# Kernel optimization log

Measured on AMD Instinct MI355X. Metric: run time of the kernel, lower is better.

The kernel has to match this reference:

```python
import jax, jax.numpy as jnp
import numpy as np

ROPE_BASE = 10000.0


def apply_rope(x, start_pos):
    # x: (b, s, n, d) -- interleaved-pair rotary embedding (LLaMA style)
    b, s, n, d = x.shape
    inv_freq = 1.0 / (ROPE_BASE ** (jnp.arange(0, d, 2, dtype=jnp.float32) / d))  # (d/2,)
    pos = jnp.arange(start_pos, start_pos + s, dtype=jnp.float32)                 # (s,)
    ang = pos[:, None] * inv_freq[None, :]                                        # (s, d/2)
    cos = jnp.cos(ang)[None, :, None, :]  # (1, s, 1, d/2)
    sin = jnp.sin(ang)[None, :, None, :]
    x1 = x[..., 0::2]
    x2 = x[..., 1::2]
    out = jnp.stack([x1 * cos - x2 * sin, x1 * sin + x2 * cos], axis=-1)
    return out.reshape(b, s, n, d).astype(x.dtype)


def setup_inputs() -> dict:
    key = jax.random.key(0)
    k1, k2, k3, k4 = jax.random.split(key, 4)
    b, n, s, d = 4, 32, 512, 128
    max_b, n_mem = 4, 4096
    return {
        "q": jax.random.normal(k1, (b, n, s, d), dtype=jnp.float32),
        "k": jax.random.normal(k2, (b, n, s, d), dtype=jnp.float32),
        "v": jax.random.normal(k3, (b, n, s, d), dtype=jnp.float32),
        "mem_kv": jax.random.normal(k4, (2, max_b, n_mem, n, d), dtype=jnp.float32),
        "start_pos": 2048,
    }


def reference(q, k, v, mem_kv, start_pos):
    b, n, s, d = q.shape
    # view_in: (b n s d) -> (b s n d)
    q_ = jnp.transpose(q, (0, 2, 1, 3))
    k_ = jnp.transpose(k, (0, 2, 1, 3))
    v_ = jnp.transpose(v, (0, 2, 1, 3))
    # rotary on q, k with absolute positions offset by start_pos
    q_ = apply_rope(q_, start_pos)
    k_ = apply_rope(k_, start_pos)
    # KV-cache write + read
    mem_k = mem_kv[0].at[:b, start_pos:start_pos + s].set(k_)
    mem_v = mem_kv[1].at[:b, start_pos:start_pos + s].set(v_)
    k_full = mem_k[:b, :start_pos + s]  # (b, t, n, d)
    v_full = mem_v[:b, :start_pos + s]
    # view_out: (b s n d) -> (b n s d)
    qh = jnp.transpose(q_, (0, 2, 1, 3))
    kh = jnp.transpose(k_full, (0, 2, 1, 3))
    vh = jnp.transpose(v_full, (0, 2, 1, 3))
    scale = d ** (-0.5)
    sim = jnp.einsum('bnsd,bntd->bnst', qh, kh) * scale
    attn = jax.nn.softmax(sim, axis=-1)
    return jnp.einsum('bnst,bntd->bnsd', attn, vh)
```

## Files before the change

kernel.cpp:

```cpp
#include <hip/hip_runtime.h>

#define BB   4
#define NN   32
#define SS   512
#define DD   128
#define NMEM 4096
#define MAXB 4
#define MQ   64
#define NK   64

typedef __attribute__((ext_vector_type(8))) short short8;
typedef __attribute__((ext_vector_type(4))) short short4v;
typedef __attribute__((ext_vector_type(4))) float f32x4;

__device__ __forceinline__ ushort bf16_rne(float x) {
    unsigned u = __float_as_uint(x);
    return (ushort)((u + 0x7FFFu + ((u >> 16) & 1u)) >> 16);
}

__device__ __forceinline__ void split_bf16(float x, ushort& hi, ushort& lo) {
    ushort hb = bf16_rne(x);
    float hf = __uint_as_float(((unsigned)hb) << 16);
    hi = hb;
    lo = bf16_rne(x - hf);
}

__device__ __forceinline__ void load_kv_row(const float* __restrict__ kg,
                                            const float* __restrict__ vg,
                                            const float* __restrict__ mg,
                                            int batch, int head, int start_pos, int T,
                                            int t, int d0, float nlb,
                                            float* kb, float* vb)
{
    if (t < start_pos) {
        const float* ks = mg + (((long)batch * NMEM + t) * NN + head) * DD + d0;
        const float* vs = ks + (long)MAXB * NMEM * NN * DD;
        float4 kk = *(const float4*)ks;
        float4 vv = *(const float4*)vs;
        kb[0] = kk.x; kb[1] = kk.y; kb[2] = kk.z; kb[3] = kk.w;
        vb[0] = vv.x; vb[1] = vv.y; vb[2] = vv.z; vb[3] = vv.w;
    } else if (t < T) {
        const long off = (((long)(batch * NN + head)) * SS + (t - start_pos)) * DD + d0;
        float4 kk = *(const float4*)(kg + off);
        float4 vv = *(const float4*)(vg + off);
        float sn, cs;
        sincosf((float)t * __expf(nlb * (float)d0), &sn, &cs);
        kb[0] = kk.x * cs - kk.y * sn;
        kb[1] = kk.x * sn + kk.y * cs;
        sincosf((float)t * __expf(nlb * (float)(d0 + 2)), &sn, &cs);
        kb[2] = kk.z * cs - kk.w * sn;
        kb[3] = kk.z * sn + kk.w * cs;
        vb[0] = vv.x; vb[1] = vv.y; vb[2] = vv.z; vb[3] = vv.w;
    } else {
        kb[0] = kb[1] = kb[2] = kb[3] = 0.f;
        vb[0] = vb[1] = vb[2] = vb[3] = 0.f;
    }
}

__global__ __launch_bounds__(256)
void mra_attn_mfma(const float* __restrict__ qg,
                   const float* __restrict__ kg,
                   const float* __restrict__ vg,
                   const float* __restrict__ mg,
                   const int*  __restrict__ spp,
                   float* __restrict__ outg)
{
    const int start_pos = spp[0];
    const int T = start_pos + SS;
    const int ntiles = (T + NK - 1) / NK;

    const int qblk  = blockIdx.x;
    const int head  = blockIdx.y;
    const int batch = blockIdx.z;
    const int tid   = threadIdx.x;
    const int wv    = tid >> 6;
    const int lane  = tid & 63;
    const int h     = lane >> 4;
    const int m     = lane & 15;

    __shared__ ushort khi[NK * DD];
    __shared__ ushort klo[NK * DD];
    __shared__ ushort vts[DD * NK];

    const float nlb   = -9.210340371976184f / 128.0f;
    const float scale = 0.08838834764831845f;

    const int q0 = qblk * MQ;
#pragma unroll
    for (int p = 0; p < 8; ++p) {
        const int idx = p * 1024 + tid * 4;
        const int row = idx >> 7;
        const int col = idx & 127;
        const int pos = start_pos + q0 + row;
        float4 x = *(const float4*)(qg + (((long)(batch * NN + head)) * SS + q0 + row) * DD + col);
        float sn, cs;
        sincosf((float)pos * __expf(nlb * (float)col), &sn, &cs);
        float e0 = (x.x * cs - x.y * sn) * scale;
        float e1 = (x.x * sn + x.y * cs) * scale;
        sincosf((float)pos * __expf(nlb * (float)(col + 2)), &sn, &cs);
        float e2 = (x.z * cs - x.w * sn) * scale;
        float e3 = (x.z * sn + x.w * cs) * scale;
        ushort hh[4], ll[4];
        split_bf16(e0, hh[0], ll[0]);
        split_bf16(e1, hh[1], ll[1]);
        split_bf16(e2, hh[2], ll[2]);
        split_bf16(e3, hh[3], ll[3]);
        *(ushort4*)(&khi[row * DD + col]) = make_ushort4(hh[0], hh[1], hh[2], hh[3]);
        *(ushort4*)(&klo[row * DD + col]) = make_ushort4(ll[0], ll[1], ll[2], ll[3]);
    }
    __syncthreads();

    short8 qfh[4], qfl[4];
    {
        const ushort* qrh = &khi[(wv * 16 + m) * DD];
        const ushort* qrl = &klo[(wv * 16 + m) * DD];
#pragma unroll
        for (int dc = 0; dc < 4; ++dc) {
            qfh[dc] = *(const short8*)(qrh + dc * 32 + h * 8);
            qfl[dc] = *(const short8*)(qrl + dc * 32 + h * 8);
        }
    }
    __syncthreads();

    f32x4 acc[8];
    const f32x4 zero4 = {0.f, 0.f, 0.f, 0.f};
#pragma unroll
    for (int i = 0; i < 8; ++i) acc[i] = zero4;
    float m_run = -1e30f, l_run = 0.f;

    for (int kt = 0; kt < ntiles; ++kt) {
        const int tile0 = kt * NK;

#pragma unroll
        for (int p = 0; p < 4; ++p) {
            const int pi = p * 256 + tid;
            const int d0 = (pi & 31) * 4;
            const int t0 = (pi >> 5) * 2;
            float kA[4], vA[4], kB[4], vB[4];
            load_kv_row(kg, vg, mg, batch, head, start_pos, T, tile0 + t0,     d0, nlb, kA, vA);
            load_kv_row(kg, vg, mg, batch, head, start_pos, T, tile0 + t0 + 1, d0, nlb, kB, vB);
            {
                const int co = d0 ^ ((t0 & 7) << 3);
                ushort hh[4], ll[4];
#pragma unroll
                for (int j = 0; j < 4; ++j) split_bf16(kA[j], hh[j], ll[j]);
                *(ushort4*)(&khi[t0 * DD + co]) = make_ushort4(hh[0], hh[1], hh[2], hh[3]);
                *(ushort4*)(&klo[t0 * DD + co]) = make_ushort4(ll[0], ll[1], ll[2], ll[3]);
            }
            {
                const int t1 = t0 + 1;
                const int co = d0 ^ ((t1 & 7) << 3);
                ushort hh[4], ll[4];
#pragma unroll
                for (int j = 0; j < 4; ++j) split_bf16(kB[j], hh[j], ll[j]);
                *(ushort4*)(&khi[t1 * DD + co]) = make_ushort4(hh[0], hh[1], hh[2], hh[3]);
                *(ushort4*)(&klo[t1 * DD + co]) = make_ushort4(ll[0], ll[1], ll[2], ll[3]);
            }
#pragma unroll
            for (int j = 0; j < 4; ++j) {
                const int d = d0 + j;
                unsigned pk = (unsigned)bf16_rne(vA[j]) | ((unsigned)bf16_rne(vB[j]) << 16);
                *(unsigned*)(&vts[d * NK + (t0 ^ ((d & 15) << 2))]) = pk;
            }
        }
        __syncthreads();

        float sc[16];
#pragma unroll
        for (int c = 0; c < 4; ++c) {
            f32x4 s = zero4;
            const int krow = c * 16 + m;
            const ushort* krh = &khi[krow * DD];
            const ushort* krl = &klo[krow * DD];
            const int sw = (krow & 7) << 3;
#pragma unroll
            for (int dc = 0; dc < 4; ++dc) {
                const int o = (dc * 32 + h * 8) ^ sw;
                short8 kfh = *(const short8*)(krh + o);
                short8 kfl = *(const short8*)(krl + o);
                s = __builtin_amdgcn_mfma_f32_16x16x32_bf16(kfh, qfh[dc], s, 0, 0, 0);
                s = __builtin_amdgcn_mfma_f32_16x16x32_bf16(kfh, qfl[dc], s, 0, 0, 0);
                s = __builtin_amdgcn_mfma_f32_16x16x32_bf16(kfl, qfh[dc], s, 0, 0, 0);
            }
            if (tile0 + NK > T) {
#pragma unroll
                for (int r = 0; r < 4; ++r)
                    if (tile0 + c * 16 + h * 4 + r >= T) s[r] = -1e30f;
            }
#pragma unroll
            for (int r = 0; r < 4; ++r) sc[c * 4 + r] = s[r];
        }

        float mloc = sc[0];
#pragma unroll
        for (int i = 1; i < 16; ++i) mloc = fmaxf(mloc, sc[i]);
        mloc = fmaxf(mloc, __shfl_xor(mloc, 16));
        mloc = fmaxf(mloc, __shfl_xor(mloc, 32));
        const float mnew = fmaxf(m_run, mloc);
        float lloc = 0.f;
#pragma unroll
        for (int i = 0; i < 16; ++i) {
            float pv = __expf(sc[i] - mnew);
            sc[i] = pv;
            lloc += pv;
        }
        lloc += __shfl_xor(lloc, 16);
        lloc += __shfl_xor(lloc, 32);
        const float alpha = __expf(m_run - mnew);
        l_run = l_run * alpha + lloc;
        m_run = mnew;
#pragma unroll
        for (int db = 0; db < 8; ++db) acc[db] = acc[db] * alpha;

#pragma unroll
        for (int g = 0; g < 2; ++g) {
            short8 pf;
#pragma unroll
            for (int j = 0; j < 8; ++j) pf[j] = (short)bf16_rne(sc[g * 8 + j]);
#pragma unroll
            for (int db = 0; db < 8; ++db) {
                const int drow = db * 16 + m;
                const ushort* vr = &vts[drow * NK];
                const int sw = (drow & 15) << 2;
                short4v a0 = *(const short4v*)(vr + ((g * 32 + h * 4) ^ sw));
                short4v a1 = *(const short4v*)(vr + ((g * 32 + 16 + h * 4) ^ sw));
                short8 vf = __builtin_shufflevector(a0, a1, 0, 1, 2, 3, 4, 5, 6, 7);
                acc[db] = __builtin_amdgcn_mfma_f32_16x16x32_bf16(vf, pf, acc[db], 0, 0, 0);
            }
        }
        __syncthreads();
    }

    const float inv_l = 1.f / l_run;
    float* dst = outg + (((long)(batch * NN + head)) * SS + q0 + wv * 16 + m) * DD;
#pragma unroll
    for (int db = 0; db < 8; ++db) {
        float4 o = make_float4(acc[db][0] * inv_l, acc[db][1] * inv_l,
                               acc[db][2] * inv_l, acc[db][3] * inv_l);
        *(float4*)(dst + db * 16 + h * 4) = o;
    }
}

extern "C" void kernel_launch(void* const* d_in, const int* in_sizes, int n_in,
                              void* d_out, int out_size, void* d_ws, size_t ws_size,
                              hipStream_t stream) {
    const float* q      = (const float*)d_in[0];
    const float* k      = (const float*)d_in[1];
    const float* v      = (const float*)d_in[2];
    const float* mem_kv = (const float*)d_in[3];
    const int*   sp     = (const int*)d_in[4];
    float* out = (float*)d_out;

    dim3 grid(SS / MQ, NN, BB);
    dim3 block(256);
    hipLaunchKernelGGL(mra_attn_mfma, grid, block, 0, stream, q, k, v, mem_kv, sp, out);
}
```

Baseline: 1.174 ms.

## Double query tile per block, specialize KV staging by region, remap grid

Raises the query tile from 64 to 128 rows with 512-thread blocks, so each staged K/V tile feeds twice as many queries and global K/V traffic is halved. KV staging is templated into memory-only, new-only and mixed modes, which removes per-row branching and hoists the rope frequencies. Q rope is loaded straight into registers instead of going through LDS. The grid is flattened and remapped so the query blocks of a head run on different dispatch slots. The hi part of the bf16 split is changed to truncation. The trade-off is fewer blocks (512), higher register pressure under launch_bounds(512,4), and the trailing barrier moved to the top of the loop.

Result: faster. 1.031 ms (-12.2%).

```diff
diff --git a/kernel.cpp b/kernel.cpp
--- a/kernel.cpp
+++ b/kernel.cpp
@@ -6,8 +6,9 @@
 #define DD   128
 #define NMEM 4096
 #define MAXB 4
-#define MQ   64
+#define MQ   128
 #define NK   64
+#define VOFF ((long)MAXB * NMEM * NN * DD)
 
 typedef __attribute__((ext_vector_type(8))) short short8;
 typedef __attribute__((ext_vector_type(4))) short short4v;
@@ -19,37 +20,37 @@
 }
 
 __device__ __forceinline__ void split_bf16(float x, ushort& hi, ushort& lo) {
-    ushort hb = bf16_rne(x);
-    float hf = __uint_as_float(((unsigned)hb) << 16);
-    hi = hb;
-    lo = bf16_rne(x - hf);
-}
-
-__device__ __forceinline__ void load_kv_row(const float* __restrict__ kg,
-                                            const float* __restrict__ vg,
-                                            const float* __restrict__ mg,
-                                            int batch, int head, int start_pos, int T,
-                                            int t, int d0, float nlb,
-                                            float* kb, float* vb)
+    unsigned u = __float_as_uint(x);
+    hi = (ushort)(u >> 16);
+    lo = bf16_rne(x - __uint_as_float(u & 0xffff0000u));
+}
+
+template<int MODE>
+__device__ __forceinline__ void fetch_row(const float* __restrict__ kmem,
+                                          const float* __restrict__ knew,
+                                          const float* __restrict__ vnew,
+                                          int t, int start_pos, int T,
+                                          float fr0, float fr2,
+                                          float* kb, float* vb)
 {
-    if (t < start_pos) {
-        const float* ks = mg + (((long)batch * NMEM + t) * NN + head) * DD + d0;
-        const float* vs = ks + (long)MAXB * NMEM * NN * DD;
+    const bool from_mem = (MODE == 0) || (MODE == 2 && t < start_pos);
+    if (from_mem) {
+        const float* ks = kmem + (long)t * (NN * DD);
         float4 kk = *(const float4*)ks;
-        float4 vv = *(const float4*)vs;
+        float4 vv = *(const float4*)(ks + VOFF);
         kb[0] = kk.x; kb[1] = kk.y; kb[2] = kk.z; kb[3] = kk.w;
         vb[0] = vv.x; vb[1] = vv.y; vb[2] = vv.z; vb[3] = vv.w;
-    } else if (t < T) {
-        const long off = (((long)(batch * NN + head)) * SS + (t - start_pos)) * DD + d0;
-        float4 kk = *(const float4*)(kg + off);
-        float4 vv = *(const float4*)(vg + off);
-        float sn, cs;
-        sincosf((float)t * __expf(nlb * (float)d0), &sn, &cs);
-        kb[0] = kk.x * cs - kk.y * sn;
-        kb[1] = kk.x * sn + kk.y * cs;
-        sincosf((float)t * __expf(nlb * (float)(d0 + 2)), &sn, &cs);
-        kb[2] = kk.z * cs - kk.w * sn;
-        kb[3] = kk.z * sn + kk.w * cs;
+    } else if (MODE == 1 || t < T) {
+        const long off = (long)(t - start_pos) * DD;
+        float4 kk = *(const float4*)(knew + off);
+        float4 vv = *(const float4*)(vnew + off);
+        float sn0, cs0, sn2, cs2;
+        sincosf((float)t * fr0, &sn0, &cs0);
+        sincosf((float)t * fr2, &sn2, &cs2);
+        kb[0] = kk.x * cs0 - kk.y * sn0;
+        kb[1] = kk.x * sn0 + kk.y * cs0;
+        kb[2] = kk.z * cs2 - kk.w * sn2;
+        kb[3] = kk.z * sn2 + kk.w * cs2;
         vb[0] = vv.x; vb[1] = vv.y; vb[2] = vv.z; vb[3] = vv.w;
     } else {
         kb[0] = kb[1] = kb[2] = kb[3] = 0.f;
@@ -57,7 +58,49 @@
     }
 }
 
-__global__ __launch_bounds__(256)
+template<int MODE>
+__device__ __forceinline__ void stage_tile(const float* __restrict__ kmem,
+                                           const float* __restrict__ knew,
+                                           const float* __restrict__ vnew,
+                                           int tile0, int start_pos, int T,
+                                           int d0, int tr0, float fr0, float fr2,
+                                           ushort* __restrict__ khi,
+                                           ushort* __restrict__ klo,
+                                           ushort* __restrict__ vts)
+{
+#pragma unroll
+    for (int p = 0; p < 2; ++p) {
+        const int trr = tr0 + p * 32;
+        float kA[4], vA[4], kB[4], vB[4];
+        fetch_row<MODE>(kmem, knew, vnew, tile0 + trr,     start_pos, T, fr0, fr2, kA, vA);
+        fetch_row<MODE>(kmem, knew, vnew, tile0 + trr + 1, start_pos, T, fr0, fr2, kB, vB);
+        {
+            const int co = d0 ^ ((trr & 7) << 3);
+            ushort hh[4], ll[4];
+#pragma unroll
+            for (int j = 0; j < 4; ++j) split_bf16(kA[j], hh[j], ll[j]);
+            *(ushort4*)(&khi[trr * DD + co]) = make_ushort4(hh[0], hh[1], hh[2], hh[3]);
+            *(ushort4*)(&klo[trr * DD + co]) = make_ushort4(ll[0], ll[1], ll[2], ll[3]);
+        }
+        {
+            const int t1 = trr + 1;
+            const int co = d0 ^ ((t1 & 7) << 3);
+            ushort hh[4], ll[4];
+#pragma unroll
+            for (int j = 0; j < 4; ++j) split_bf16(kB[j], hh[j], ll[j]);
+            *(ushort4*)(&khi[t1 * DD + co]) = make_ushort4(hh[0], hh[1], hh[2], hh[3]);
+            *(ushort4*)(&klo[t1 * DD + co]) = make_ushort4(ll[0], ll[1], ll[2], ll[3]);
+        }
+#pragma unroll
+        for (int j = 0; j < 4; ++j) {
+            const int d = d0 + j;
+            unsigned pk = (unsigned)bf16_rne(vA[j]) | ((unsigned)bf16_rne(vB[j]) << 16);
+            *(unsigned*)(&vts[d * NK + (trr ^ ((d & 15) << 2))]) = pk;
+        }
+    }
+}
+
+__global__ __launch_bounds__(512, 4)
 void mra_attn_mfma(const float* __restrict__ qg,
                    const float* __restrict__ kg,
                    const float* __restrict__ vg,
@@ -69,14 +112,18 @@
     const int T = start_pos + SS;
     const int ntiles = (T + NK - 1) / NK;
 
-    const int qblk  = blockIdx.x;
-    const int head  = blockIdx.y;
-    const int batch = blockIdx.z;
-    const int tid   = threadIdx.x;
-    const int wv    = tid >> 6;
-    const int lane  = tid & 63;
-    const int h     = lane >> 4;
-    const int m     = lane & 15;
+    const int flat  = blockIdx.x;
+    const int work  = (flat & 7) * 64 + (flat >> 3);
+    const int qblk  = work & 3;
+    const int grp   = work >> 2;
+    const int head  = grp & 31;
+    const int batch = grp >> 5;
+
+    const int tid  = threadIdx.x;
+    const int wv   = tid >> 6;
+    const int lane = tid & 63;
+    const int h    = lane >> 4;
+    const int m    = lane & 15;
 
     __shared__ ushort khi[NK * DD];
     __shared__ ushort klo[NK * DD];
@@ -85,42 +132,42 @@
     const float nlb   = -9.210340371976184f / 128.0f;
     const float scale = 0.08838834764831845f;
 
-    const int q0 = qblk * MQ;
-#pragma unroll
-    for (int p = 0; p < 8; ++p) {
-        const int idx = p * 1024 + tid * 4;
-        const int row = idx >> 7;
-        const int col = idx & 127;
-        const int pos = start_pos + q0 + row;
-        float4 x = *(const float4*)(qg + (((long)(batch * NN + head)) * SS + q0 + row) * DD + col);
-        float sn, cs;
-        sincosf((float)pos * __expf(nlb * (float)col), &sn, &cs);
-        float e0 = (x.x * cs - x.y * sn) * scale;
-        float e1 = (x.x * sn + x.y * cs) * scale;
-        sincosf((float)pos * __expf(nlb * (float)(col + 2)), &sn, &cs);
-        float e2 = (x.z * cs - x.w * sn) * scale;
-        float e3 = (x.z * sn + x.w * cs) * scale;
-        ushort hh[4], ll[4];
-        split_bf16(e0, hh[0], ll[0]);
-        split_bf16(e1, hh[1], ll[1]);
-        split_bf16(e2, hh[2], ll[2]);
-        split_bf16(e3, hh[3], ll[3]);
-        *(ushort4*)(&khi[row * DD + col]) = make_ushort4(hh[0], hh[1], hh[2], hh[3]);
-        *(ushort4*)(&klo[row * DD + col]) = make_ushort4(ll[0], ll[1], ll[2], ll[3]);
-    }
-    __syncthreads();
-
+    const int q0   = qblk * MQ;
+    const int qrow = q0 + wv * 16 + m;
+    const float pos = (float)(start_pos + qrow);
+    const float* qbase = qg + (((long)(batch * NN + head)) * SS + qrow) * DD;
     short8 qfh[4], qfl[4];
-    {
-        const ushort* qrh = &khi[(wv * 16 + m) * DD];
-        const ushort* qrl = &klo[(wv * 16 + m) * DD];
-#pragma unroll
-        for (int dc = 0; dc < 4; ++dc) {
-            qfh[dc] = *(const short8*)(qrh + dc * 32 + h * 8);
-            qfl[dc] = *(const short8*)(qrl + dc * 32 + h * 8);
-        }
-    }
-    __syncthreads();
+#pragma unroll
+    for (int dc = 0; dc < 4; ++dc) {
+        const int cb = dc * 32 + h * 8;
+        float4 xa = *(const float4*)(qbase + cb);
+        float4 xb = *(const float4*)(qbase + cb + 4);
+        float e[8];
+        float f, sn, cs;
+        f = __expf(nlb * (float)cb);       sincosf(pos * f, &sn, &cs);
+        e[0] = (xa.x * cs - xa.y * sn) * scale;  e[1] = (xa.x * sn + xa.y * cs) * scale;
+        f = __expf(nlb * (float)(cb + 2)); sincosf(pos * f, &sn, &cs);
+        e[2] = (xa.z * cs - xa.w * sn) * scale;  e[3] = (xa.z * sn + xa.w * cs) * scale;
+        f = __expf(nlb * (float)(cb + 4)); sincosf(pos * f, &sn, &cs);
+        e[4] = (xb.x * cs - xb.y * sn) * scale;  e[5] = (xb.x * sn + xb.y * cs) * scale;
+        f = __expf(nlb * (float)(cb + 6)); sincosf(pos * f, &sn, &cs);
+        e[6] = (xb.z * cs - xb.w * sn) * scale;  e[7] = (xb.z * sn + xb.w * cs) * scale;
+#pragma unroll
+        for (int j = 0; j < 8; ++j) {
+            ushort hh, ll;
+            split_bf16(e[j], hh, ll);
+            qfh[dc][j] = (short)hh;
+            qfl[dc][j] = (short)ll;
+        }
+    }
+
+    const int d0  = (tid & 31) * 4;
+    const int tr0 = (tid >> 5) * 2;
+    const float fr0 = __expf(nlb * (float)d0);
+    const float fr2 = __expf(nlb * (float)(d0 + 2));
+    const float* kmem = mg + (long)batch * NMEM * NN * DD + head * DD + d0;
+    const float* knew = kg + (((long)(batch * NN + head)) * SS) * DD + d0;
+    const float* vnew = vg + (((long)(batch * NN + head)) * SS) * DD + d0;
 
     f32x4 acc[8];
     const f32x4 zero4 = {0.f, 0.f, 0.f, 0.f};
@@ -130,39 +177,14 @@
 
     for (int kt = 0; kt < ntiles; ++kt) {
         const int tile0 = kt * NK;
-
-#pragma unroll
-        for (int p = 0; p < 4; ++p) {
-            const int pi = p * 256 + tid;
-            const int d0 = (pi & 31) * 4;
-            const int t0 = (pi >> 5) * 2;
-            float kA[4], vA[4], kB[4], vB[4];
-            load_kv_row(kg, vg, mg, batch, head, start_pos, T, tile0 + t0,     d0, nlb, kA, vA);
-            load_kv_row(kg, vg, mg, batch, head, start_pos, T, tile0 + t0 + 1, d0, nlb, kB, vB);
-            {
-                const int co = d0 ^ ((t0 & 7) << 3);
-                ushort hh[4], ll[4];
-#pragma unroll
-                for (int j = 0; j < 4; ++j) split_bf16(kA[j], hh[j], ll[j]);
-                *(ushort4*)(&khi[t0 * DD + co]) = make_ushort4(hh[0], hh[1], hh[2], hh[3]);
-                *(ushort4*)(&klo[t0 * DD + co]) = make_ushort4(ll[0], ll[1], ll[2], ll[3]);
-            }
-            {
-                const int t1 = t0 + 1;
-                const int co = d0 ^ ((t1 & 7) << 3);
-                ushort hh[4], ll[4];
-#pragma unroll
-                for (int j = 0; j < 4; ++j) split_bf16(kB[j], hh[j], ll[j]);
-                *(ushort4*)(&khi[t1 * DD + co]) = make_ushort4(hh[0], hh[1], hh[2], hh[3]);
-                *(ushort4*)(&klo[t1 * DD + co]) = make_ushort4(ll[0], ll[1], ll[2], ll[3]);
-            }
-#pragma unroll
-            for (int j = 0; j < 4; ++j) {
-                const int d = d0 + j;
-                unsigned pk = (unsigned)bf16_rne(vA[j]) | ((unsigned)bf16_rne(vB[j]) << 16);
-                *(unsigned*)(&vts[d * NK + (t0 ^ ((d & 15) << 2))]) = pk;
-            }
-        }
+        __syncthreads();
+
+        if (tile0 + NK <= start_pos)
+            stage_tile<0>(kmem, knew, vnew, tile0, start_pos, T, d0, tr0, fr0, fr2, khi, klo, vts);
+        else if (tile0 >= start_pos && tile0 + NK <= T)
+            stage_tile<1>(kmem, knew, vnew, tile0, start_pos, T, d0, tr0, fr0, fr2, khi, klo, vts);
+        else
+            stage_tile<2>(kmem, knew, vnew, tile0, start_pos, T, d0, tr0, fr0, fr2, khi, klo, vts);
         __syncthreads();
 
         float sc[16];
@@ -228,11 +250,10 @@
                 acc[db] = __builtin_amdgcn_mfma_f32_16x16x32_bf16(vf, pf, acc[db], 0, 0, 0);
             }
         }
-        __syncthreads();
     }
 
     const float inv_l = 1.f / l_run;
-    float* dst = outg + (((long)(batch * NN + head)) * SS + q0 + wv * 16 + m) * DD;
+    float* dst = outg + (((long)(batch * NN + head)) * SS + qrow) * DD;
 #pragma unroll
     for (int db = 0; db < 8; ++db) {
         float4 o = make_float4(acc[db][0] * inv_l, acc[db][1] * inv_l,
@@ -251,7 +272,7 @@
     const int*   sp     = (const int*)d_in[4];
     float* out = (float*)d_out;
 
-    dim3 grid(SS / MQ, NN, BB);
-    dim3 block(256);
+    dim3 grid(512);
+    dim3 block(512);
     hipLaunchKernelGGL(mra_attn_mfma, grid, block, 0, stream, q, k, v, mem_kv, sp, out);
 }
```
